# Kernel tuning notes

Measured on AMD Instinct MI355X. Metric: run time of the kernel, lower is better.

Reference implementation:

```python
import jax, jax.numpy as jnp
import numpy as np

N = 100000      # nodes
E = 1600000     # edges (avg degree 16)
F_IN = 128      # num_features
H = 128         # hidden_channels
OUT = 64        # out_channels


def _glorot(key, shape):
    lim = float(np.sqrt(6.0 / (shape[0] + shape[1])))
    return jax.random.uniform(key, shape, jnp.float32, -lim, lim)


def setup_inputs() -> dict:
    key = jax.random.key(0)
    ks = jax.random.split(key, 5)
    x = jax.random.normal(ks[0], (N, F_IN), jnp.float32)
    edge_index = jax.random.randint(ks[1], (2, E), 0, N, dtype=jnp.int64)
    W1 = _glorot(ks[2], (F_IN, H)); b1 = jnp.zeros((H,), jnp.float32)
    W2 = _glorot(ks[3], (H, H));    b2 = jnp.zeros((H,), jnp.float32)
    W3 = _glorot(ks[4], (H, OUT));  b3 = jnp.zeros((OUT,), jnp.float32)
    return {"x": x, "edge_index": edge_index,
            "W1": W1, "b1": b1, "W2": W2, "b2": b2, "W3": W3, "b3": b3}


def _gcn_conv(h, src, dst, norm, W, b, n):
    # PyG GCNConv: linear transform, then sym-normalized scatter aggregation, then bias
    h = h @ W                                   # [N, d_out]
    msg = h[src] * norm[:, None]                # gather + scale, [E+N, d_out]
    agg = jax.ops.segment_sum(msg, dst, num_segments=n)
    return agg + b


def reference(x, edge_index, W1, b1, W2, b2, W3, b3):
    n = x.shape[0]
    # add self-loops (GCNConv default add_self_loops=True)
    loop = jnp.arange(n, dtype=edge_index.dtype)
    src = jnp.concatenate([edge_index[0], loop])
    dst = jnp.concatenate([edge_index[1], loop])
    # symmetric normalization deg^-1/2[src] * deg^-1/2[dst]
    deg = jax.ops.segment_sum(jnp.ones_like(dst, x.dtype), dst, num_segments=n)
    dinv = jnp.where(deg > 0, jax.lax.rsqrt(deg), 0.0)
    norm = dinv[src] * dinv[dst]

    h = jax.nn.relu(_gcn_conv(x, src, dst, norm, W1, b1, n))  # dropout p=0 -> no-op
    h = jax.nn.relu(_gcn_conv(h, src, dst, norm, W2, b2, n))
    h = _gcn_conv(h, src, dst, norm, W3, b3, n)
    return jax.nn.log_softmax(h, axis=1)
```

## Files before the change

kernel.cpp:

```cpp
#include <hip/hip_runtime.h>
#include <stdint.h>
#include <math.h>

#define FIN 128

typedef __attribute__((ext_vector_type(8))) short short8v;
typedef __attribute__((ext_vector_type(4))) float float4v;
typedef __attribute__((ext_vector_type(2))) float float2v;

__device__ __forceinline__ uint32_t f2_to_bf2(float x, float y) {
    uint32_t r;
    asm("v_cvt_pk_bf16_f32 %0, %1, %2" : "=v"(r) : "v"(x), "v"(y));
    return r;
}
__device__ __forceinline__ unsigned short f_to_bf(float x) {
    union { float f; uint32_t i; } a;
    a.f = x;
    uint32_t u = a.i + 0x7FFF + ((a.i >> 16) & 1);
    return (unsigned short)(u >> 16);
}
__device__ __forceinline__ void acc16_fp8_pk(float2v* acc2, uint4 v) {
    uint32_t us[4] = {v.x, v.y, v.z, v.w};
#pragma unroll
    for (int q = 0; q < 4; ++q) {
        acc2[q * 2 + 0] += __builtin_amdgcn_cvt_pk_f32_fp8(us[q], false);
        acc2[q * 2 + 1] += __builtin_amdgcn_cvt_pk_f32_fp8(us[q], true);
    }
}

template <int CTRL>
__device__ __forceinline__ float dppmov(float x) {
    int i = __builtin_bit_cast(int, x);
    int r = __builtin_amdgcn_update_dpp(i, i, CTRL, 0xF, 0xF, false);
    return __builtin_bit_cast(float, r);
}
__device__ __forceinline__ float swz16f(float x) {
    int r = __builtin_amdgcn_ds_swizzle(__builtin_bit_cast(int, x), 0x401F);
    return __builtin_bit_cast(float, r);
}

__device__ __forceinline__ int edge_at(const void* ei, long long idx, int is32) {
    return is32 ? ((const int*)ei)[idx] : (int)((const long long*)ei)[idx];
}

#define SP_CHUNK 4096
__global__ __launch_bounds__(256) void splitA_kernel(const void* __restrict__ ei,
                                                     int* __restrict__ gCnt,
                                                     uint32_t* __restrict__ buf1,
                                                     int E, int capS) {
    __shared__ int hist[16];
    __shared__ int gbase[16];
    __shared__ int lflag;
    int t = threadIdx.x;
    if (t < 16) hist[t] = 0;
    if (t == 0) lflag = 0;
    long long base = (long long)blockIdx.x * SP_CHUNK;
    __syncthreads();
    {
        long long e = base + t;
        if (e < E && ((const int*)ei)[2 * e + 1] != 0) atomicOr(&lflag, 1);
    }
    __syncthreads();
    int is32 = lflag;
    uint32_t lrec[16], rec[16];
#pragma unroll
    for (int j = 0; j < 16; ++j) {
        long long e = base + t + j * 256;
        if (e < E) {
            int s = edge_at(ei, e, is32);
            int d = edge_at(ei, (long long)E + e, is32);
            int b = d >> 13;
            int lofs = atomicAdd(&hist[b], 1);
            lrec[j] = ((uint32_t)lofs << 4) | (uint32_t)b;
            rec[j] = ((uint32_t)s << 13) | (uint32_t)(d & 8191);
        } else
            lrec[j] = 0xFFFFFFFFu;
    }
    __syncthreads();
    if (t < 16) gbase[t] = atomicAdd(&gCnt[t], hist[t]);
    __syncthreads();
#pragma unroll
    for (int j = 0; j < 16; ++j) {
        if (lrec[j] != 0xFFFFFFFFu) {
            int b = lrec[j] & 15;
            int pos = gbase[b] + (int)(lrec[j] >> 4);
            if (pos < capS) buf1[(size_t)b * capS + pos] = rec[j];
        }
    }
}

__global__ __launch_bounds__(256) void splitB_kernel(const int* __restrict__ gCnt,
                                                     const uint32_t* __restrict__ buf1,
                                                     int* __restrict__ cnt2,
                                                     uint32_t* __restrict__ buf2,
                                                     int capS, int cap2, int NB) {
    __shared__ int hist[128];
    __shared__ int gbase[128];
    int t = threadIdx.x;
    int s = blockIdx.y;
    if (t < 128) hist[t] = 0;
    __syncthreads();
    int m = gCnt[s];
    if (m > capS) m = capS;
    long long base = (long long)blockIdx.x * SP_CHUNK;
    uint32_t lrec[16], r32[16];
#pragma unroll
    for (int j = 0; j < 16; ++j) {
        long long i = base + t + j * 256;
        if (i < m) {
            uint32_t r = buf1[(size_t)s * capS + i];
            int d13 = (int)(r & 8191u);
            int sub = d13 >> 6;
            int lofs = atomicAdd(&hist[sub], 1);
            lrec[j] = ((uint32_t)lofs << 7) | (uint32_t)sub;
            r32[j] = ((r >> 13) << 6) | (uint32_t)(d13 & 63);
        } else
            lrec[j] = 0xFFFFFFFFu;
    }
    __syncthreads();
    if (t < 128) {
        int g = s * 128 + t;
        gbase[t] = (g < NB) ? atomicAdd(&cnt2[g], hist[t]) : 0;
    }
    __syncthreads();
#pragma unroll
    for (int j = 0; j < 16; ++j) {
        if (lrec[j] != 0xFFFFFFFFu) {
            int sub = lrec[j] & 127;
            int pos = gbase[sub] + (int)(lrec[j] >> 7);
            if (pos < cap2) buf2[(size_t)(s * 128 + sub) * cap2 + pos] = r32[j];
        }
    }
}

__global__ __launch_bounds__(256) void binBC_kernel(const int* __restrict__ cnt2,
                                                    const uint32_t* __restrict__ buf2,
                                                    int* __restrict__ cnt,
                                                    float* __restrict__ dinv,
                                                    int* __restrict__ rowstart,
                                                    int* __restrict__ col,
                                                    int n, int cap2) {
    __shared__ int h[64];
    __shared__ int rowst[64];
    __shared__ int cur[64];
    __shared__ int sc[64];
    int bin = blockIdx.x;
    int t = threadIdx.x;
    if (t < 64) {
        h[t] = (bin * 64 + t < n) ? 1 : 0;
        cur[t] = 1;
    }
    __syncthreads();
    int m = cnt2[bin];
    if (m > cap2) m = cap2;
    const uint32_t* buf = buf2 + (size_t)bin * cap2;
    for (int i = t; i < m; i += 256) atomicAdd(&h[buf[i] & 63], 1);
    __syncthreads();
    int c = 0, pc = 0;
    if (t < 64) { c = h[t]; pc = (c + 7) & ~7; sc[t] = pc; }
    __syncthreads();
    for (int off = 1; off < 64; off <<= 1) {
        int v = 0;
        if (t < 64 && t >= off) v = sc[t - off];
        __syncthreads();
        if (t < 64) sc[t] += v;
        __syncthreads();
    }
    if (t < 64) {
        int node = bin * 64 + t;
        int base = bin * cap2;
        int st = base + sc[t] - pc;
        rowst[t] = st;
        if (node < n) {
            cnt[node] = c;
            dinv[node] = rsqrtf((float)c);
            rowstart[node] = st;
            col[st] = node;
            for (int k = c; k < pc; ++k) col[st + k] = n;
        }
    }
    __syncthreads();
    for (int i = t; i < m; i += 256) {
        uint32_t rec = buf[i];
        int d6 = rec & 63;
        int off = atomicAdd(&cur[d6], 1);
        col[rowst[d6] + off] = (int)(rec >> 6);
    }
}

__global__ __launch_bounds__(256) void wconv_all(const float* __restrict__ W1,
                                                 const float* __restrict__ W2,
                                                 const float* __restrict__ W3,
                                                 unsigned short* __restrict__ Wf1,
                                                 unsigned short* __restrict__ Wf2,
                                                 unsigned short* __restrict__ Wf3) {
    int idx = blockIdx.x * 256 + threadIdx.x;
    const float* W;
    unsigned short* Wf;
    int NCOL, base;
    if (idx < 2048)      { W = W1; Wf = Wf1; NCOL = 128; base = idx; }
    else if (idx < 4096) { W = W2; Wf = Wf2; NCOL = 128; base = idx - 2048; }
    else if (idx < 5120) { W = W3; Wf = Wf3; NCOL = 64;  base = idx - 4096; }
    else return;
    int f = base >> 6, l = base & 63;
    int ct = f >> 2, ks = f & 3;
    int nn = ct * 16 + (l & 15);
    int k0 = ks * 32 + (l >> 4) * 8;
    uint32_t pk[4];
#pragma unroll
    for (int j = 0; j < 4; ++j) {
        float a = W[(size_t)(k0 + 2 * j) * NCOL + nn];
        float b = W[(size_t)(k0 + 2 * j + 1) * NCOL + nn];
        pk[j] = f2_to_bf2(a, b);
    }
    uint4 v = make_uint4(pk[0], pk[1], pk[2], pk[3]);
    ((uint4*)Wf)[base] = v;
}

template <int NCOL, int A_FP32, int OUT_FP8>
__global__ __launch_bounds__(256) void gemm_mfma(const void* __restrict__ Av,
                                                 const unsigned short* __restrict__ Wf,
                                                 const float* __restrict__ dinv,
                                                 void* __restrict__ Cv, int n) {
    __shared__ unsigned short lds[NCOL * 128];
    const int t = threadIdx.x;
    if (blockIdx.x == 0 && t < NCOL / 4)
        ((uint32_t*)Cv)[(size_t)n * (NCOL / 4) + t] = 0;
    for (int i = t; i < NCOL * 16; i += 256)
        ((uint4*)lds)[i] = ((const uint4*)Wf)[i];
    __syncthreads();

    const int wave = t >> 6, lane = t & 63;
    const int row0 = blockIdx.x * 64 + wave * 16;
    const int m = lane & 15, quad = lane >> 4;
    int arow = row0 + m;
    if (arow >= n) arow = n - 1;

    short8v a[4];
    if (A_FP32) {
        const float* A = (const float*)Av;
#pragma unroll
        for (int ks = 0; ks < 4; ++ks) {
            float4 lo = *(const float4*)(A + (size_t)arow * 128 + ks * 32 + quad * 8);
            float4 hi = *(const float4*)(A + (size_t)arow * 128 + ks * 32 + quad * 8 + 4);
            union { short8v v; uint32_t u[4]; } pk;
            pk.u[0] = f2_to_bf2(lo.x, lo.y);
            pk.u[1] = f2_to_bf2(lo.z, lo.w);
            pk.u[2] = f2_to_bf2(hi.x, hi.y);
            pk.u[3] = f2_to_bf2(hi.z, hi.w);
            a[ks] = pk.v;
        }
    } else {
        const unsigned short* A = (const unsigned short*)Av;
#pragma unroll
        for (int ks = 0; ks < 4; ++ks)
            a[ks] = *(const short8v*)(A + (size_t)arow * 128 + ks * 32 + quad * 8);
    }

    const int cr0 = row0 + quad * 4;
    float ds[4];
#pragma unroll
    for (int r = 0; r < 4; ++r) {
        int gr = cr0 + r;
        ds[r] = (gr < n) ? dinv[gr] : 0.0f;
    }
#pragma unroll
    for (int ct = 0; ct < NCOL / 16; ++ct) {
        float4v acc = {0.0f, 0.0f, 0.0f, 0.0f};
#pragma unroll
        for (int ks = 0; ks < 4; ++ks) {
            int f = ct * 4 + ks;
            short8v b = *(const short8v*)(lds + ((size_t)(f * 64 + lane)) * 8);
            acc = __builtin_amdgcn_mfma_f32_16x16x32_bf16(a[ks], b, acc, 0, 0, 0);
        }
#pragma unroll
        for (int r = 0; r < 4; ++r) {
            int gr = cr0 + r;
            if (gr < n) {
                float val = acc[r] * ds[r];
                if (OUT_FP8) {
                    int u = __builtin_amdgcn_cvt_pk_fp8_f32(val, val, 0, false);
                    ((unsigned char*)Cv)[(size_t)gr * NCOL + ct * 16 + m] =
                        (unsigned char)(u & 0xFF);
                } else {
                    ((unsigned short*)Cv)[(size_t)gr * NCOL + ct * 16 + m] = f_to_bf(val);
                }
            }
        }
    }
}

__global__ __launch_bounds__(256) void agg_relu_128_fp8(
        const uint32_t* __restrict__ T8, const int* __restrict__ rowstart,
        const int* __restrict__ cnt, const int* __restrict__ col,
        const float* __restrict__ dinv, const float* __restrict__ bias,
        uint32_t* __restrict__ outHb, int n) {
    int wid = blockIdx.x * 4 + (threadIdx.x >> 6);
    int lane = threadIdx.x & 63;
    int j = lane & 7, slot = (lane >> 3) & 3, sel = lane >> 5;
    int nodeA = wid * 2;
    int node = nodeA + sel;
    if (nodeA >= n) return;
    bool valid = node < n;
    int nd = valid ? node : nodeA;
    int start = rowstart[nd];
    int c = cnt[nd];
    int nit = valid ? (((c + 7) & ~7) >> 3) : 0;

    float2v acc2[8];
#pragma unroll
    for (int k = 0; k < 8; ++k) acc2[k] = (float2v){0.0f, 0.0f};
    const uint4* T4 = (const uint4*)T8;
    int bp = start + slot;
    int s00 = col[bp +  0], s01 = col[bp +  4];
    int s10 = col[bp +  8], s11 = col[bp + 12];
    int s20 = col[bp + 16], s21 = col[bp + 20];
    int s30 = col[bp + 24], s31 = col[bp + 28];
    s00 = (0 < nit) ? s00 : n;  s01 = (0 < nit) ? s01 : n;
    s10 = (1 < nit) ? s10 : n;  s11 = (1 < nit) ? s11 : n;
    s20 = (2 < nit) ? s20 : n;  s21 = (2 < nit) ? s21 : n;
    s30 = (3 < nit) ? s30 : n;  s31 = (3 < nit) ? s31 : n;
    uint4 v00 = T4[(size_t)s00 * 8 + j], v01 = T4[(size_t)s01 * 8 + j];
    uint4 v10 = T4[(size_t)s10 * 8 + j], v11 = T4[(size_t)s11 * 8 + j];
    uint4 v20 = T4[(size_t)s20 * 8 + j], v21 = T4[(size_t)s21 * 8 + j];
    uint4 v30 = T4[(size_t)s30 * 8 + j], v31 = T4[(size_t)s31 * 8 + j];
    acc16_fp8_pk(acc2, v00); acc16_fp8_pk(acc2, v01);
    acc16_fp8_pk(acc2, v10); acc16_fp8_pk(acc2, v11);
    acc16_fp8_pk(acc2, v20); acc16_fp8_pk(acc2, v21);
    acc16_fp8_pk(acc2, v30); acc16_fp8_pk(acc2, v31);
    for (int s = 4; s < nit; ++s) {
        int a0 = col[bp + s * 8], a1 = col[bp + s * 8 + 4];
        uint4 w0 = T4[(size_t)a0 * 8 + j];
        uint4 w1 = T4[(size_t)a1 * 8 + j];
        acc16_fp8_pk(acc2, w0);
        acc16_fp8_pk(acc2, w1);
    }
    float* acc = (float*)acc2;
#pragma unroll
    for (int k = 0; k < 16; ++k) acc[k] += dppmov<0x128>(acc[k]);
#pragma unroll
    for (int k = 0; k < 16; ++k) acc[k] += swz16f(acc[k]);
    if (slot == 0 && valid) {
        float di = dinv[node];
        const float4* b4 = (const float4*)bias;
        float r[16];
#pragma unroll
        for (int q = 0; q < 4; ++q) {
            float4 bb = b4[j * 4 + q];
            r[q * 4 + 0] = fmaxf(di * acc[q * 4 + 0] + bb.x, 0.0f);
            r[q * 4 + 1] = fmaxf(di * acc[q * 4 + 1] + bb.y, 0.0f);
            r[q * 4 + 2] = fmaxf(di * acc[q * 4 + 2] + bb.z, 0.0f);
            r[q * 4 + 3] = fmaxf(di * acc[q * 4 + 3] + bb.w, 0.0f);
        }
        uint4 o0, o1;
        o0.x = f2_to_bf2(r[0], r[1]);   o0.y = f2_to_bf2(r[2], r[3]);
        o0.z = f2_to_bf2(r[4], r[5]);   o0.w = f2_to_bf2(r[6], r[7]);
        o1.x = f2_to_bf2(r[8], r[9]);   o1.y = f2_to_bf2(r[10], r[11]);
        o1.z = f2_to_bf2(r[12], r[13]); o1.w = f2_to_bf2(r[14], r[15]);
        *(uint4*)(outHb + (size_t)node * 64 + j * 8) = o0;
        *(uint4*)(outHb + (size_t)node * 64 + j * 8 + 4) = o1;
    }
}

__global__ __launch_bounds__(256) void agg_lsm_64_fp8(
        const uint32_t* __restrict__ T8, const int* __restrict__ rowstart,
        const int* __restrict__ cnt, const int* __restrict__ col,
        const float* __restrict__ dinv, const float* __restrict__ bias,
        float* __restrict__ out, int n) {
    int wid = blockIdx.x * 4 + (threadIdx.x >> 6);
    int lane = threadIdx.x & 63;
    int j = lane & 3, slot = (lane >> 2) & 7, sel = lane >> 5;
    int nodeA = wid * 2;
    int node = nodeA + sel;
    if (nodeA >= n) return;
    bool valid = node < n;
    int nd = valid ? node : nodeA;
    int start = rowstart[nd];
    int c = cnt[nd];
    int nit = valid ? (((c + 7) & ~7) >> 3) : 0;

    float2v acc2[8];
#pragma unroll
    for (int k = 0; k < 8; ++k) acc2[k] = (float2v){0.0f, 0.0f};
    const uint4* T4 = (const uint4*)T8;
    int bp = start + slot;
    int a0 = col[bp +  0];
    int a1 = col[bp +  8];
    int a2 = col[bp + 16];
    int a3 = col[bp + 24];
    a0 = (0 < nit) ? a0 : n;
    a1 = (1 < nit) ? a1 : n;
    a2 = (2 < nit) ? a2 : n;
    a3 = (3 < nit) ? a3 : n;
    uint4 v0 = T4[(size_t)a0 * 4 + j];
    uint4 v1 = T4[(size_t)a1 * 4 + j];
    uint4 v2 = T4[(size_t)a2 * 4 + j];
    uint4 v3 = T4[(size_t)a3 * 4 + j];
    acc16_fp8_pk(acc2, v0);
    acc16_fp8_pk(acc2, v1);
    acc16_fp8_pk(acc2, v2);
    acc16_fp8_pk(acc2, v3);
    for (int s = 4; s < nit; ++s) {
        int aa = col[bp + s * 8];
        uint4 w = T4[(size_t)aa * 4 + j];
        acc16_fp8_pk(acc2, w);
    }
    float* acc = (float*)acc2;
#pragma unroll
    for (int k = 0; k < 16; ++k) acc[k] += dppmov<0x124>(acc[k]);
#pragma unroll
    for (int k = 0; k < 16; ++k) acc[k] += dppmov<0x128>(acc[k]);
#pragma unroll
    for (int k = 0; k < 16; ++k) acc[k] += swz16f(acc[k]);
    float di = dinv[nd];
    const float4* b4 = (const float4*)bias;
    float r[16];
#pragma unroll
    for (int q = 0; q < 4; ++q) {
        float4 bb = b4[j * 4 + q];
        r[q * 4 + 0] = di * acc[q * 4 + 0] + bb.x;
        r[q * 4 + 1] = di * acc[q * 4 + 1] + bb.y;
        r[q * 4 + 2] = di * acc[q * 4 + 2] + bb.z;
        r[q * 4 + 3] = di * acc[q * 4 + 3] + bb.w;
    }
    float m0 = fmaxf(fmaxf(r[0], r[1]), fmaxf(r[2], r[3]));
    float m1 = fmaxf(fmaxf(r[4], r[5]), fmaxf(r[6], r[7]));
    float m2 = fmaxf(fmaxf(r[8], r[9]), fmaxf(r[10], r[11]));
    float m3 = fmaxf(fmaxf(r[12], r[13]), fmaxf(r[14], r[15]));
    float m = fmaxf(fmaxf(m0, m1), fmaxf(m2, m3));
    m = fmaxf(m, dppmov<0xB1>(m));
    m = fmaxf(m, dppmov<0x4E>(m));
    float e0 = __expf(r[0] - m) + __expf(r[1] - m) + __expf(r[2] - m) +
               __expf(r[3] - m);
    float e1 = __expf(r[4] - m) + __expf(r[5] - m) + __expf(r[6] - m) +
               __expf(r[7] - m);
    float e2 = __expf(r[8] - m) + __expf(r[9] - m) + __expf(r[10] - m) +
               __expf(r[11] - m);
    float e3 = __expf(r[12] - m) + __expf(r[13] - m) + __expf(r[14] - m) +
               __expf(r[15] - m);
    float ss = (e0 + e1) + (e2 + e3);
    ss += dppmov<0xB1>(ss);
    ss += dppmov<0x4E>(ss);
    float lg = m + __logf(ss);
    if (slot == 0 && valid) {
#pragma unroll
        for (int q = 0; q < 4; ++q) {
            float4 o = make_float4(r[q * 4 + 0] - lg, r[q * 4 + 1] - lg,
                                   r[q * 4 + 2] - lg, r[q * 4 + 3] - lg);
            *(float4*)(out + (size_t)node * 64 + j * 16 + q * 4) = o;
        }
    }
}

extern "C" void kernel_launch(void* const* d_in, const int* in_sizes, int n_in,
                              void* d_out, int out_size, void* d_ws, size_t ws_size,
                              hipStream_t stream) {
    const float* x  = (const float*)d_in[0];
    const void*  ei = d_in[1];
    const float* W1 = (const float*)d_in[2];
    const float* b1 = (const float*)d_in[3];
    const float* W2 = (const float*)d_in[4];
    const float* b2 = (const float*)d_in[5];
    const float* W3 = (const float*)d_in[6];
    const float* b3 = (const float*)d_in[7];
    float* out = (float*)d_out;

    const int n = in_sizes[0] / FIN;
    const int E = in_sizes[1] / 2;

    char* p = (char*)d_ws;
    auto carve = [&](size_t bytes) {
        char* q = p;
        p += (bytes + 255) & ~(size_t)255;
        return q;
    };
    const int NB = (n + 63) / 64;
    const int NS = (n + 8191) / 8192;

    long long meanS = (long long)E * 8192 / n;
    int capS = (int)(meanS + 8 * (long long)sqrt((double)meanS) + 1024);
    capS = (capS + 15) & ~15;
    long long mean2 = (long long)E * 64 / n;
    int cap2 = (int)(mean2 + 8 * (long long)sqrt((double)mean2) + 1152);
    cap2 = (cap2 + 15) & ~15;

    int*   cnt      = (int*)carve((size_t)n * 4);
    int*   rowstart = (int*)carve((size_t)n * 4);
    float* dinv     = (float*)carve((size_t)n * 4);
    int*   colb     = (int*)carve(((size_t)NB * cap2 + 4096) * 4);
    int*   gCnt     = (int*)carve((size_t)(16 + NB) * 4);
    int*   cnt2     = gCnt + 16;
    size_t Tbytes = (size_t)n * 128 + 256;
    size_t Hbytes = (size_t)n * 128 * 2;
    char*  TH = carve(Tbytes + Hbytes);
    void*  T  = (void*)TH;
    unsigned short* Hb = (unsigned short*)(TH + Tbytes);
    unsigned short* Wf1 = (unsigned short*)carve(128 * 128 * 2);
    unsigned short* Wf2 = (unsigned short*)carve(128 * 128 * 2);
    unsigned short* Wf3 = (unsigned short*)carve(128 * 64 * 2);

    size_t buf1B = ((size_t)NS * capS * 4 + 255) & ~(size_t)255;
    uint32_t* buf1 = (uint32_t*)TH;
    uint32_t* buf2 = (uint32_t*)(TH + buf1B);
    size_t avail2 = (Tbytes + Hbytes > buf1B) ? (Tbytes + Hbytes - buf1B) : 0;
    size_t maxc2 = avail2 / ((size_t)NB * 4);
    if ((size_t)cap2 > maxc2) cap2 = (int)maxc2;

    hipMemsetAsync(gCnt, 0, (size_t)(16 + NB) * 4, stream);

    const int gagg2 = ((n + 1) / 2 + 3) / 4;
    const int ggemm = (n + 63) / 64;
    const int gsplitA = (E + SP_CHUNK - 1) / SP_CHUNK;
    const int gsplitBx = (capS + SP_CHUNK - 1) / SP_CHUNK;

    splitA_kernel<<<gsplitA, 256, 0, stream>>>(ei, gCnt, buf1, E, capS);
    splitB_kernel<<<dim3(gsplitBx, NS), 256, 0, stream>>>(gCnt, buf1, cnt2, buf2, capS,
                                                          cap2, NB);
    binBC_kernel<<<NB, 256, 0, stream>>>(cnt2, buf2, cnt, dinv, rowstart, colb, n,
                                         cap2);
    wconv_all<<<20, 256, 0, stream>>>(W1, W2, W3, Wf1, Wf2, Wf3);

    gemm_mfma<128, 1, 1><<<ggemm, 256, 0, stream>>>(x, Wf1, dinv, T, n);
    agg_relu_128_fp8<<<gagg2, 256, 0, stream>>>((const uint32_t*)T, rowstart, cnt,
                                                colb, dinv, b1, (uint32_t*)Hb, n);
    gemm_mfma<128, 0, 1><<<ggemm, 256, 0, stream>>>(Hb, Wf2, dinv, T, n);
    agg_relu_128_fp8<<<gagg2, 256, 0, stream>>>((const uint32_t*)T, rowstart, cnt,
                                                colb, dinv, b2, (uint32_t*)Hb, n);
    gemm_mfma<64, 0, 1><<<ggemm, 256, 0, stream>>>(Hb, Wf3, dinv, T, n);
    agg_lsm_64_fp8<<<gagg2, 256, 0, stream>>>((const uint32_t*)T, rowstart, cnt, colb,
                                              dinv, b3, out, n);
}
```

Baseline: 281.9 us.

## Stage splitB scatter in LDS for coalesced writes; fold weight conversion into splitA

splitB now runs a prefix scan over per-bucket counts and reorders its records in shared memory by sub-bucket. It then writes them to global memory in contiguous runs, replacing scattered per-record stores. This should improve write coalescing, at the cost of about 20KB of extra LDS, which may lower occupancy, plus a few extra barriers. Separately, the weight bf16 conversion moves into extra blocks of splitA, removing one kernel launch.

```diff
diff --git a/kernel.cpp b/kernel.cpp
--- a/kernel.cpp
+++ b/kernel.cpp
@@ -44,14 +44,39 @@
 }
 
 #define SP_CHUNK 4096
-__global__ __launch_bounds__(256) void splitA_kernel(const void* __restrict__ ei,
-                                                     int* __restrict__ gCnt,
-                                                     uint32_t* __restrict__ buf1,
-                                                     int E, int capS) {
+__global__ __launch_bounds__(256) void splitA_kernel(
+        const void* __restrict__ ei, int* __restrict__ gCnt,
+        uint32_t* __restrict__ buf1, int E, int capS, int nA,
+        const float* __restrict__ W1, const float* __restrict__ W2,
+        const float* __restrict__ W3, unsigned short* __restrict__ Wf1,
+        unsigned short* __restrict__ Wf2, unsigned short* __restrict__ Wf3) {
     __shared__ int hist[16];
     __shared__ int gbase[16];
     __shared__ int lflag;
     int t = threadIdx.x;
+    if (blockIdx.x >= nA) {
+        int idx = (blockIdx.x - nA) * 256 + t;
+        const float* W;
+        unsigned short* Wf;
+        int NCOL, base;
+        if (idx < 2048)      { W = W1; Wf = Wf1; NCOL = 128; base = idx; }
+        else if (idx < 4096) { W = W2; Wf = Wf2; NCOL = 128; base = idx - 2048; }
+        else if (idx < 5120) { W = W3; Wf = Wf3; NCOL = 64;  base = idx - 4096; }
+        else return;
+        int f = base >> 6, l = base & 63;
+        int ct = f >> 2, ks = f & 3;
+        int nn = ct * 16 + (l & 15);
+        int k0 = ks * 32 + (l >> 4) * 8;
+        uint32_t pk[4];
+#pragma unroll
+        for (int j = 0; j < 4; ++j) {
+            float a = W[(size_t)(k0 + 2 * j) * NCOL + nn];
+            float b = W[(size_t)(k0 + 2 * j + 1) * NCOL + nn];
+            pk[j] = f2_to_bf2(a, b);
+        }
+        ((uint4*)Wf)[base] = make_uint4(pk[0], pk[1], pk[2], pk[3]);
+        return;
+    }
     if (t < 16) hist[t] = 0;
     if (t == 0) lflag = 0;
     long long base = (long long)blockIdx.x * SP_CHUNK;
@@ -95,7 +120,10 @@
                                                      uint32_t* __restrict__ buf2,
                                                      int capS, int cap2, int NB) {
     __shared__ int hist[128];
+    __shared__ int sbase[128];
     __shared__ int gbase[128];
+    __shared__ uint32_t ordrec[SP_CHUNK];
+    __shared__ unsigned char ordsub[SP_CHUNK];
     int t = threadIdx.x;
     int s = blockIdx.y;
     if (t < 128) hist[t] = 0;
@@ -118,18 +146,38 @@
             lrec[j] = 0xFFFFFFFFu;
     }
     __syncthreads();
+    if (t < 128) sbase[t] = hist[t];
+    __syncthreads();
+    for (int off = 1; off < 128; off <<= 1) {
+        int v = 0;
+        if (t < 128 && t >= off) v = sbase[t - off];
+        __syncthreads();
+        if (t < 128) sbase[t] += v;
+        __syncthreads();
+    }
     if (t < 128) {
         int g = s * 128 + t;
-        gbase[t] = (g < NB) ? atomicAdd(&cnt2[g], hist[t]) : 0;
+        gbase[t] = (g < NB && hist[t] > 0) ? atomicAdd(&cnt2[g], hist[t]) : 0;
+        sbase[t] -= hist[t];
     }
     __syncthreads();
 #pragma unroll
     for (int j = 0; j < 16; ++j) {
         if (lrec[j] != 0xFFFFFFFFu) {
             int sub = lrec[j] & 127;
-            int pos = gbase[sub] + (int)(lrec[j] >> 7);
-            if (pos < cap2) buf2[(size_t)(s * 128 + sub) * cap2 + pos] = r32[j];
-        }
+            int pos = sbase[sub] + (int)(lrec[j] >> 7);
+            ordrec[pos] = r32[j];
+            ordsub[pos] = (unsigned char)sub;
+        }
+    }
+    __syncthreads();
+    int mloc = (int)(m - base);
+    if (mloc > SP_CHUNK) mloc = SP_CHUNK;
+    if (mloc < 0) mloc = 0;
+    for (int i = t; i < mloc; i += 256) {
+        int sub = ordsub[i];
+        int gpos = gbase[sub] + (i - sbase[sub]);
+        if (gpos < cap2) buf2[(size_t)(s * 128 + sub) * cap2 + gpos] = ordrec[i];
     }
 }
 
@@ -186,35 +234,6 @@
         int off = atomicAdd(&cur[d6], 1);
         col[rowst[d6] + off] = (int)(rec >> 6);
     }
-}
-
-__global__ __launch_bounds__(256) void wconv_all(const float* __restrict__ W1,
-                                                 const float* __restrict__ W2,
-                                                 const float* __restrict__ W3,
-                                                 unsigned short* __restrict__ Wf1,
-                                                 unsigned short* __restrict__ Wf2,
-                                                 unsigned short* __restrict__ Wf3) {
-    int idx = blockIdx.x * 256 + threadIdx.x;
-    const float* W;
-    unsigned short* Wf;
-    int NCOL, base;
-    if (idx < 2048)      { W = W1; Wf = Wf1; NCOL = 128; base = idx; }
-    else if (idx < 4096) { W = W2; Wf = Wf2; NCOL = 128; base = idx - 2048; }
-    else if (idx < 5120) { W = W3; Wf = Wf3; NCOL = 64;  base = idx - 4096; }
-    else return;
-    int f = base >> 6, l = base & 63;
-    int ct = f >> 2, ks = f & 3;
-    int nn = ct * 16 + (l & 15);
-    int k0 = ks * 32 + (l >> 4) * 8;
-    uint32_t pk[4];
-#pragma unroll
-    for (int j = 0; j < 4; ++j) {
-        float a = W[(size_t)(k0 + 2 * j) * NCOL + nn];
-        float b = W[(size_t)(k0 + 2 * j + 1) * NCOL + nn];
-        pk[j] = f2_to_bf2(a, b);
-    }
-    uint4 v = make_uint4(pk[0], pk[1], pk[2], pk[3]);
-    ((uint4*)Wf)[base] = v;
 }
 
 template <int NCOL, int A_FP32, int OUT_FP8>
@@ -513,12 +532,12 @@
     const int gsplitA = (E + SP_CHUNK - 1) / SP_CHUNK;
     const int gsplitBx = (capS + SP_CHUNK - 1) / SP_CHUNK;
 
-    splitA_kernel<<<gsplitA, 256, 0, stream>>>(ei, gCnt, buf1, E, capS);
+    splitA_kernel<<<gsplitA + 20, 256, 0, stream>>>(ei, gCnt, buf1, E, capS, gsplitA,
+                                                    W1, W2, W3, Wf1, Wf2, Wf3);
     splitB_kernel<<<dim3(gsplitBx, NS), 256, 0, stream>>>(gCnt, buf1, cnt2, buf2, capS,
                                                           cap2, NB);
     binBC_kernel<<<NB, 256, 0, stream>>>(cnt2, buf2, cnt, dinv, rowstart, colb, n,
                                          cap2);
-    wconv_all<<<20, 256, 0, stream>>>(W1, W2, W3, Wf1, Wf2, Wf3);
 
     gemm_mfma<128, 1, 1><<<ggemm, 256, 0, stream>>>(x, Wf1, dinv, T, n);
     agg_relu_128_fp8<<<gagg2, 256, 0, stream>>>((const uint32_t*)T, rowstart, cnt,
```

New measurement: 278.3 us, median of 2. Within noise of the previous version (-1.3%).
